# Kernel optimization log

Measured on AMD Instinct MI355X. Metric: run time of the kernel, lower is better.

## Reference

```python
import jax, jax.numpy as jnp
import numpy as np

B, N, D = 16, 4096, 6
NUM_CENTERS, K = 1024, 32
EPS = 1e-5


def setup_inputs() -> dict:
    key = jax.random.key(0)
    ks = jax.random.split(key, 6)
    xyz = jax.random.uniform(ks[0], (B, N, 3), dtype=jnp.float32)
    features = jax.random.normal(ks[1], (B, N, D), dtype=jnp.float32)
    W1 = jax.random.normal(ks[2], (3 + D, 64), dtype=jnp.float32) * 0.1
    W2 = jax.random.normal(ks[3], (64, 64), dtype=jnp.float32) * 0.1
    W3 = jax.random.normal(ks[4], (64, 128), dtype=jnp.float32) * 0.1
    return {
        "xyz": xyz, "features": features,
        "W1": W1, "g1": jnp.ones((64,)), "b1": jnp.zeros((64,)),
        "W2": W2, "g2": jnp.ones((64,)), "b2": jnp.zeros((64,)),
        "W3": W3, "g3": jnp.ones((128,)), "b3": jnp.zeros((128,)),
    }


def square_distance(a, b):
    # a: [B,S,3], b: [B,N,3] -> [B,S,N] squared euclidean distance
    d2 = (jnp.sum(a * a, -1)[:, :, None]
          + jnp.sum(b * b, -1)[:, None, :]
          - 2.0 * jnp.einsum('bsc,bnc->bsn', a, b))
    return jnp.maximum(d2, 0.0)


def farthest_point_sample(xyz, num_centers):
    # xyz: [B,N,3] -> centers_idx: [B,S]. First center fixed at index 0
    # (original uses a random first index; deterministic here).
    Bn = xyz.shape[0]
    batch = jnp.arange(Bn)
    first = jnp.zeros((Bn,), jnp.int32)
    d0 = jnp.sum((xyz - xyz[batch, first][:, None, :]) ** 2, -1)  # [B,N]

    def step(dist_closest, _):
        idx = jnp.argmax(dist_closest, axis=1).astype(jnp.int32)  # [B]
        c = xyz[batch, idx]                                        # [B,3]
        d = jnp.sum((xyz - c[:, None, :]) ** 2, -1)                # [B,N]
        return jnp.minimum(dist_closest, d), idx

    _, rest = jax.lax.scan(step, d0, None, length=num_centers - 1)  # [S-1,B]
    return jnp.concatenate([first[:, None], rest.T], axis=1)        # [B,S]


def gather_bsk(points, idx):
    # points: [B,N,C], idx: [B,S,K] -> [B,S,K,C]
    Bn = points.shape[0]
    return points[jnp.arange(Bn)[:, None, None], idx]


def conv_bn_relu(x, W, g, b):
    # 1x1 conv (channel matmul) + training-mode BatchNorm (biased var) + ReLU
    x = jnp.einsum('bskc,co->bsko', x, W)
    m = jnp.mean(x, axis=(0, 1, 2))
    v = jnp.var(x, axis=(0, 1, 2))
    return jax.nn.relu((x - m) * jax.lax.rsqrt(v + EPS) * g + b)


def reference(xyz, features, W1, g1, b1, W2, g2, b2, W3, g3, b3):
    Bn = xyz.shape[0]
    batch = jnp.arange(Bn)
    centers_idx = farthest_point_sample(xyz, NUM_CENTERS)          # [B,S]
    centers_xyz = xyz[batch[:, None], centers_idx]                  # [B,S,3]

    # kNN grouping: [B,S,N] distance matrix, top-K smallest
    d2 = square_distance(centers_xyz, xyz)
    _, group_idx = jax.lax.top_k(-d2, K)                            # [B,S,K]

    group_xyz = gather_bsk(xyz, group_idx) - centers_xyz[:, :, None, :]
    group_feat = gather_bsk(features, group_idx)
    group = jnp.concatenate([group_xyz, group_feat], axis=-1)       # [B,S,K,3+D]

    x = conv_bn_relu(group, W1, g1, b1)
    x = conv_bn_relu(x, W2, g2, b2)
    x = conv_bn_relu(x, W3, g3, b3)
    centers_features = jnp.max(x, axis=2)                           # [B,S,C_out]
    return centers_xyz, centers_features
```

## Files before the change

kernel.cpp:

```cpp
#include <hip/hip_runtime.h>

#define BN_   16
#define NPTS  4096
#define DFEAT 6
#define SCTR  1024
#define KNN   32
#define RTOT  (BN_*SCTR*KNN)
#define EPSV  1e-5f
#define RNF   524288.0f
#define NREP  64

__device__ __forceinline__ float fmulx(float a, float b){ return __fmul_rn(a,b); }
__device__ __forceinline__ float faddx(float a, float b){ return __fadd_rn(a,b); }
__device__ __forceinline__ float fsubx(float a, float b){ return __fsub_rn(a,b); }
__device__ __forceinline__ float sq3x(float x, float y, float z){
  return faddx(faddx(fmulx(x,x), fmulx(y,y)), fmulx(z,z));
}
__device__ __forceinline__ float dot3fma(float ax, float ay, float az,
                                         float bx, float by, float bz){
  return __fmaf_rn(az, bz, __fmaf_rn(ay, by, __fmul_rn(ax, bx)));
}

__device__ __forceinline__ unsigned fkey(float f){
  unsigned u = __float_as_uint(f);
  return (u & 0x80000000u) ? ~u : (u | 0x80000000u);
}
__device__ __forceinline__ float funkey(unsigned k){
  return (k & 0x80000000u) ? __uint_as_float(k & 0x7fffffffu) : __uint_as_float(~k);
}

template<int CTRL>
__device__ __forceinline__ unsigned dpp_mv(unsigned v){
  return (unsigned)__builtin_amdgcn_update_dpp((int)v, (int)v, CTRL, 0xf, 0xf, false);
}
__device__ __forceinline__ unsigned wave_umax_b(unsigned v){
  unsigned o;
  o=dpp_mv<0x111>(v); v=v>o?v:o;
  o=dpp_mv<0x112>(v); v=v>o?v:o;
  o=dpp_mv<0x114>(v); v=v>o?v:o;
  o=dpp_mv<0x118>(v); v=v>o?v:o;
  o=dpp_mv<0x142>(v); v=v>o?v:o;
  o=dpp_mv<0x143>(v); v=v>o?v:o;
  return (unsigned)__builtin_amdgcn_readlane((int)v, 63);
}
__device__ __forceinline__ unsigned wave_umin_b(unsigned v){
  unsigned o;
  o=dpp_mv<0x111>(v); v=v<o?v:o;
  o=dpp_mv<0x112>(v); v=v<o?v:o;
  o=dpp_mv<0x114>(v); v=v<o?v:o;
  o=dpp_mv<0x118>(v); v=v<o?v:o;
  o=dpp_mv<0x142>(v); v=v<o?v:o;
  o=dpp_mv<0x143>(v); v=v<o?v:o;
  return (unsigned)__builtin_amdgcn_readlane((int)v, 63);
}

__global__ __launch_bounds__(256) void k_fps(const float* __restrict__ xyz,
                                             float* __restrict__ cxyz){
  const int b = blockIdx.x, tid = threadIdx.x;
  const int wave = tid>>6, lane = tid&63;
  const float* X = xyz + (size_t)b*NPTS*3;
  __shared__ float Xl[NPTS*3];
  __shared__ float Cl[SCTR*3];
  __shared__ unsigned long long slot[2][4];
  for(int i=tid;i<NPTS*3;i+=256) Xl[i]=X[i];
  __syncthreads();
  float px[16],py[16],pz[16],mind[16];
  const float c0x=Xl[0], c0y=Xl[1], c0z=Xl[2];
#pragma unroll
  for(int t=0;t<16;t++){
    const int j = lane + 64*(wave*16+t);
    px[t]=Xl[j*3]; py[t]=Xl[j*3+1]; pz[t]=Xl[j*3+2];
    mind[t]=sq3x(fsubx(px[t],c0x), fsubx(py[t],c0y), fsubx(pz[t],c0z));
  }
  if(tid==0){ Cl[0]=c0x; Cl[1]=c0y; Cl[2]=c0z; }
  float bv=-1.0f; int bj=0x7fffffff;
#pragma unroll
  for(int t=0;t<16;t++){
    const int j = lane + 64*(wave*16+t);
    if(mind[t]>bv){ bv=mind[t]; bj=j; }
  }
  for(int it=1; it<SCTR; ++it){
    const unsigned uv = __float_as_uint(bv);
    const unsigned M  = wave_umax_b(uv);
    const unsigned nj = (uv == M) ? ~(unsigned)bj : 0u;
    const unsigned NJ = wave_umax_b(nj);
    if(lane==0) slot[it&1][wave] = ((unsigned long long)M<<32) | NJ;
    __syncthreads();
    unsigned long long k0=slot[it&1][0], k1=slot[it&1][1],
                       k2=slot[it&1][2], k3=slot[it&1][3];
    unsigned long long ka = k0>k1?k0:k1;
    unsigned long long kb = k2>k3?k2:k3;
    unsigned long long kw = ka>kb?ka:kb;
    const int w = (int)(~(unsigned)kw);
    const float cx=Xl[w*3], cy=Xl[w*3+1], cz=Xl[w*3+2];
    if(tid==0){ Cl[it*3]=cx; Cl[it*3+1]=cy; Cl[it*3+2]=cz; }
    bv=-1.0f; bj=0x7fffffff;
#pragma unroll
    for(int t=0;t<16;t++){
      float d = sq3x(fsubx(px[t],cx), fsubx(py[t],cy), fsubx(pz[t],cz));
      float nm = fminf(mind[t], d);
      mind[t]=nm;
      const int j = lane + 64*(wave*16+t);
      if(nm>bv){ bv=nm; bj=j; }
    }
  }
  __syncthreads();
  float* O = cxyz + (size_t)b*SCTR*3;
  for(int i=tid;i<SCTR*3;i+=256) O[i]=Cl[i];
}

__global__ __launch_bounds__(256) void k_select(const float* __restrict__ xyz,
                                                const float* __restrict__ cxyz,
                                                int* __restrict__ gidx){
  const int lane = threadIdx.x & 63;
  const int cid  = blockIdx.x*4 + (threadIdx.x>>6);
  const int b = cid>>10;
  const float* X = xyz + (size_t)b*NPTS*3;
  const float* C = cxyz + (size_t)cid*3;
  const float cx=C[0], cy=C[1], cz=C[2];
  const float a2 = sq3x(cx,cy,cz);
  float d[64];
#pragma unroll
  for(int t=0;t<64;t++){
    int j = lane + (t<<6);
    float x=X[j*3], y=X[j*3+1], z=X[j*3+2];
    float b2 = sq3x(x,y,z);
    float dt = dot3fma(cx,cy,cz, x,y,z);
    float dd = fsubx(faddx(a2,b2), fmulx(2.0f,dt));
    d[t] = fmaxf(dd, 0.0f);
  }
  unsigned long long taken = 0ull;
  int* out = gidx + (size_t)cid*KNN;
#pragma unroll 1
  for(int r=0;r<KNN;r++){
    float mv = 3.0e38f; int mt = 63;
#pragma unroll
    for(int t=0;t<64;t++){
      if(!(taken & (1ull<<t)) && d[t] < mv){ mv = d[t]; mt = t; }
    }
    const unsigned um = __float_as_uint(mv);
    const unsigned Mw = wave_umin_b(um);
    const unsigned jc = (um == Mw) ? (unsigned)(lane + (mt<<6)) : 0xffffffffu;
    const unsigned WJ = wave_umin_b(jc);
    if(lane == (int)(WJ & 63u)){
      out[r] = (int)WJ;
      taken |= (1ull << (WJ >> 6));
    }
  }
}

__device__ __forceinline__ void stage_in(float* INt, int rbase,
                                         const float* __restrict__ xyz,
                                         const float* __restrict__ feat,
                                         const float* __restrict__ cxyz,
                                         const int* __restrict__ gidx){
  const int tid = threadIdx.x;
  const int row = tid>>2, sub = tid&3;
  const int r  = rbase + row;
  const int bb = r>>15, ss=(r>>5)&1023;
  const int idx = gidx[r];
  if(sub==0){
    const float* P = xyz  + ((size_t)bb*NPTS + idx)*3;
    const float* C = cxyz + ((size_t)(bb*SCTR)+ss)*3;
    INt[0*68+row] = P[0]-C[0];
    INt[1*68+row] = P[1]-C[1];
    INt[2*68+row] = P[2]-C[2];
  }else{
    const float* F = feat + ((size_t)bb*NPTS + idx)*6;
    const int c = (sub-1)*2;
    INt[(3+c)*68+row] = F[c];
    INt[(4+c)*68+row] = F[c+1];
  }
}

__device__ __forceinline__ void gemm1(const float* INt, const float* __restrict__ W1,
                                      int rt, int ct, float acc[4][4]){
#pragma unroll
  for(int i=0;i<4;i++)
#pragma unroll
    for(int j=0;j<4;j++) acc[i][j]=0.f;
#pragma unroll
  for(int c=0;c<9;c++){
    const float4 a = *(const float4*)&INt[c*68 + rt*4];
    const float4 w = *(const float4*)&W1[c*64 + ct*4];
    const float av[4]={a.x,a.y,a.z,a.w}, wv[4]={w.x,w.y,w.z,w.w};
#pragma unroll
    for(int i=0;i<4;i++)
#pragma unroll
      for(int j=0;j<4;j++) acc[i][j] += av[i]*wv[j];
  }
}

__device__ __forceinline__ float fold_rep(const float* __restrict__ pstats, int off){
  float s=0.f;
#pragma unroll 8
  for(int c=0;c<NREP;c++) s += pstats[c*512 + off];
  return s;
}

__global__ __launch_bounds__(256) void k_stats1(const float* __restrict__ xyz,
                                                const float* __restrict__ feat,
                                                const float* __restrict__ cxyz,
                                                const int* __restrict__ gidx,
                                                const float* __restrict__ W1,
                                                float* __restrict__ pstats){
  __shared__ __align__(16) float INt[9*68];
  __shared__ float sb[64], qb[64];
  const int tid=threadIdx.x;
  if(tid<64){ sb[tid]=0.f; qb[tid]=0.f; }
  stage_in(INt, blockIdx.x*64, xyz, feat, cxyz, gidx);
  __syncthreads();
  const int rt=tid&15, ct=tid>>4;
  float acc[4][4];
  gemm1(INt, W1, rt, ct, acc);
#pragma unroll
  for(int j=0;j<4;j++){
    float s=0.f, q=0.f;
#pragma unroll
    for(int i=0;i<4;i++){ float v=acc[i][j]; s+=v; q+=v*v; }
    atomicAdd(&sb[ct*4+j], s); atomicAdd(&qb[ct*4+j], q);
  }
  __syncthreads();
  if(tid<64){
    float* ps = pstats + (size_t)(blockIdx.x & (NREP-1))*512;
    atomicAdd(&ps[tid], sb[tid]); atomicAdd(&ps[64+tid], qb[tid]);
  }
}

template<bool WRITEZ>
__device__ __forceinline__ void stats2_body(const float* xyz, const float* feat,
                                            const float* cxyz, const int* gidx,
                                            const float* W1, const float* g1,
                                            const float* b1, const float* __restrict__ W2,
                                            float* pstats, float* Z2){
  __shared__ __align__(16) float INt[9*68];
  __shared__ __align__(16) float A1t[64*68];
  __shared__ float af1A[64], af1B[64];
  __shared__ float sb[64], qb[64];
  const int tid=threadIdx.x;
  if(tid<64){
    float sm = fold_rep(pstats, tid);
    float sq = fold_rep(pstats, 64+tid);
    float m  = sm/RNF;
    float vv = sq/RNF - m*m;
    float A  = rsqrtf(vv+EPSV)*g1[tid];
    af1A[tid]=A; af1B[tid]=b1[tid]-m*A;
    sb[tid]=0.f; qb[tid]=0.f;
  }
  stage_in(INt, blockIdx.x*64, xyz, feat, cxyz, gidx);
  __syncthreads();
  const int rt=tid&15, ct=tid>>4;
  float acc1[4][4];
  gemm1(INt, W1, rt, ct, acc1);
#pragma unroll
  for(int j=0;j<4;j++){
    const int o=ct*4+j; const float A=af1A[o], Bc=af1B[o];
#pragma unroll
    for(int i=0;i<4;i++) A1t[o*68 + rt*4+i] = fmaxf(acc1[i][j]*A+Bc, 0.f);
  }
  __syncthreads();
  float acc2[4][4];
#pragma unroll
  for(int i=0;i<4;i++)
#pragma unroll
    for(int j=0;j<4;j++) acc2[i][j]=0.f;
#pragma unroll
  for(int c=0;c<64;c++){
    const float4 a = *(const float4*)&A1t[c*68 + rt*4];
    const float4 w = *(const float4*)&W2[c*64 + ct*4];
    const float av[4]={a.x,a.y,a.z,a.w}, wv[4]={w.x,w.y,w.z,w.w};
#pragma unroll
    for(int i=0;i<4;i++)
#pragma unroll
      for(int j=0;j<4;j++) acc2[i][j] += av[i]*wv[j];
  }
  if(WRITEZ){
#pragma unroll
    for(int i=0;i<4;i++){
      float4 v = make_float4(acc2[i][0],acc2[i][1],acc2[i][2],acc2[i][3]);
      *(float4*)&Z2[((size_t)blockIdx.x*64 + rt*4+i)*64 + ct*4] = v;
    }
  }
#pragma unroll
  for(int j=0;j<4;j++){
    float s=0.f, q=0.f;
#pragma unroll
    for(int i=0;i<4;i++){ float v=acc2[i][j]; s+=v; q+=v*v; }
    atomicAdd(&sb[ct*4+j], s); atomicAdd(&qb[ct*4+j], q);
  }
  __syncthreads();
  if(tid<64){
    float* ps = pstats + (size_t)(blockIdx.x & (NREP-1))*512;
    atomicAdd(&ps[128+tid], sb[tid]); atomicAdd(&ps[192+tid], qb[tid]);
  }
}

__global__ __launch_bounds__(256) void k_stats2(const float* __restrict__ xyz,
                                                const float* __restrict__ feat,
                                                const float* __restrict__ cxyz,
                                                const int* __restrict__ gidx,
                                                const float* __restrict__ W1,
                                                const float* __restrict__ g1,
                                                const float* __restrict__ b1,
                                                const float* __restrict__ W2,
                                                float* __restrict__ pstats){
  stats2_body<false>(xyz,feat,cxyz,gidx,W1,g1,b1,W2,pstats,nullptr);
}
__global__ __launch_bounds__(256) void k_stats2m(const float* __restrict__ xyz,
                                                 const float* __restrict__ feat,
                                                 const float* __restrict__ cxyz,
                                                 const int* __restrict__ gidx,
                                                 const float* __restrict__ W1,
                                                 const float* __restrict__ g1,
                                                 const float* __restrict__ b1,
                                                 const float* __restrict__ W2,
                                                 float* __restrict__ pstats,
                                                 float* __restrict__ Z2){
  stats2_body<true>(xyz,feat,cxyz,gidx,W1,g1,b1,W2,pstats,Z2);
}

__global__ __launch_bounds__(256) void k_layer3(const float* __restrict__ xyz,
                                                const float* __restrict__ feat,
                                                const float* __restrict__ cxyz,
                                                const int* __restrict__ gidx,
                                                const float* __restrict__ W1,
                                                const float* __restrict__ g1,
                                                const float* __restrict__ b1,
                                                const float* __restrict__ W2,
                                                const float* __restrict__ g2,
                                                const float* __restrict__ b2,
                                                const float* __restrict__ W3,
                                                float* __restrict__ pstats,
                                                float* __restrict__ premax){
  __shared__ __align__(16) float INt[9*68];
  __shared__ __align__(16) float A1t[64*68];
  __shared__ float af1A[64], af1B[64], af2A[64], af2B[64];
  __shared__ unsigned mx[256];
  __shared__ float s3b[256], q3b[256];
  const int tid=threadIdx.x;
  if(tid<64){
    float sm = fold_rep(pstats, tid);
    float sq = fold_rep(pstats, 64+tid);
    float m  = sm/RNF;
    float vv = sq/RNF - m*m;
    float A  = rsqrtf(vv+EPSV)*g1[tid];
    af1A[tid]=A; af1B[tid]=b1[tid]-m*A;
    float sm2 = fold_rep(pstats, 128+tid);
    float sq2 = fold_rep(pstats, 192+tid);
    float m2 = sm2/RNF;
    float v2 = sq2/RNF - m2*m2;
    float A2 = rsqrtf(v2+EPSV)*g2[tid];
    af2A[tid]=A2; af2B[tid]=b2[tid]-m2*A2;
  }
  mx[tid]=0u; s3b[tid]=0.f; q3b[tid]=0.f;
  stage_in(INt, blockIdx.x*64, xyz, feat, cxyz, gidx);
  __syncthreads();
  const int rt=tid&15, ct=tid>>4;
  float acc1[4][4];
  gemm1(INt, W1, rt, ct, acc1);
#pragma unroll
  for(int j=0;j<4;j++){
    const int o=ct*4+j; const float A=af1A[o], Bc=af1B[o];
#pragma unroll
    for(int i=0;i<4;i++) A1t[o*68 + rt*4+i] = fmaxf(acc1[i][j]*A+Bc, 0.f);
  }
  __syncthreads();
  float acc2[4][4];
#pragma unroll
  for(int i=0;i<4;i++)
#pragma unroll
    for(int j=0;j<4;j++) acc2[i][j]=0.f;
#pragma unroll
  for(int c=0;c<64;c++){
    const float4 a = *(const float4*)&A1t[c*68 + rt*4];
    const float4 w = *(const float4*)&W2[c*64 + ct*4];
    const float av[4]={a.x,a.y,a.z,a.w}, wv[4]={w.x,w.y,w.z,w.w};
#pragma unroll
    for(int i=0;i<4;i++)
#pragma unroll
      for(int j=0;j<4;j++) acc2[i][j] += av[i]*wv[j];
  }
  float a2v[4][4];
#pragma unroll
  for(int j=0;j<4;j++){
    const int o=ct*4+j; const float A=af2A[o], Bc=af2B[o];
#pragma unroll
    for(int i=0;i<4;i++) a2v[i][j]=fmaxf(acc2[i][j]*A+Bc, 0.f);
  }
  __syncthreads();
#pragma unroll
  for(int j=0;j<4;j++)
#pragma unroll
    for(int i=0;i<4;i++) A1t[(ct*4+j)*68 + rt*4+i] = a2v[i][j];
  __syncthreads();
  float acc3[4][8];
#pragma unroll
  for(int i=0;i<4;i++)
#pragma unroll
    for(int j=0;j<8;j++) acc3[i][j]=0.f;
#pragma unroll
  for(int c=0;c<64;c++){
    const float4 a  = *(const float4*)&A1t[c*68 + rt*4];
    const float4 w0 = *(const float4*)&W3[c*128 + ct*8];
    const float4 w1 = *(const float4*)&W3[c*128 + ct*8 + 4];
    const float av[4]={a.x,a.y,a.z,a.w};
    const float wv[8]={w0.x,w0.y,w0.z,w0.w,w1.x,w1.y,w1.z,w1.w};
#pragma unroll
    for(int i=0;i<4;i++)
#pragma unroll
      for(int j=0;j<8;j++) acc3[i][j] += av[i]*wv[j];
  }
  const int g = rt>>3;
#pragma unroll
  for(int j=0;j<8;j++){
    const int o=ct*8+j;
    float lm=acc3[0][j], s=0.f, q=0.f;
#pragma unroll
    for(int i=0;i<4;i++){ float v=acc3[i][j]; lm=fmaxf(lm,v); s+=v; q+=v*v; }
    atomicMax(&mx[g*128+o], fkey(lm));
    atomicAdd(&s3b[g*128+o], s);
    atomicAdd(&q3b[g*128+o], q);
  }
  __syncthreads();
  {
    const int gg=tid>>7, o=tid&127;
    const int cid = blockIdx.x*2+gg;
    premax[(size_t)cid*128+o] = funkey(mx[tid]);
  }
  if(tid<128){
    float* ps = pstats + (size_t)(blockIdx.x & (NREP-1))*512;
    atomicAdd(&ps[256+tid], s3b[tid]+s3b[128+tid]);
    atomicAdd(&ps[384+tid], q3b[tid]+q3b[128+tid]);
  }
}

__global__ __launch_bounds__(256) void k_layer3z(const float* __restrict__ Z2,
                                                 const float* __restrict__ g2,
                                                 const float* __restrict__ b2,
                                                 const float* __restrict__ W3,
                                                 float* __restrict__ pstats,
                                                 float* __restrict__ premax){
  __shared__ __align__(16) float A2t[64*68];
  __shared__ float af2A[64], af2B[64];
  __shared__ unsigned mx[256];
  __shared__ float s3b[256], q3b[256];
  const int tid=threadIdx.x;
  if(tid<64){
    float sm2 = fold_rep(pstats, 128+tid);
    float sq2 = fold_rep(pstats, 192+tid);
    float m2 = sm2/RNF;
    float v2 = sq2/RNF - m2*m2;
    float A2 = rsqrtf(v2+EPSV)*g2[tid];
    af2A[tid]=A2; af2B[tid]=b2[tid]-m2*A2;
  }
  mx[tid]=0u; s3b[tid]=0.f; q3b[tid]=0.f;
  __syncthreads();
  {
    const int row = tid>>2, cq = (tid&3)*16;
    const float* zr = Z2 + ((size_t)blockIdx.x*64 + row)*64 + cq;
    const float4 z0 = *(const float4*)(zr);
    const float4 z1 = *(const float4*)(zr+4);
    const float4 z2 = *(const float4*)(zr+8);
    const float4 z3 = *(const float4*)(zr+12);
    const float zz[16]={z0.x,z0.y,z0.z,z0.w, z1.x,z1.y,z1.z,z1.w,
                        z2.x,z2.y,z2.z,z2.w, z3.x,z3.y,z3.z,z3.w};
#pragma unroll
    for(int u=0;u<16;u++){
      const int c = cq+u;
      A2t[c*68+row] = fmaxf(zz[u]*af2A[c]+af2B[c], 0.f);
    }
  }
  __syncthreads();
  const int rt=tid&15, ct=tid>>4;
  float acc3[4][8];
#pragma unroll
  for(int i=0;i<4;i++)
#pragma unroll
    for(int j=0;j<8;j++) acc3[i][j]=0.f;
#pragma unroll
  for(int c=0;c<64;c++){
    const float4 a  = *(const float4*)&A2t[c*68 + rt*4];
    const float4 w0 = *(const float4*)&W3[c*128 + ct*8];
    const float4 w1 = *(const float4*)&W3[c*128 + ct*8 + 4];
    const float av[4]={a.x,a.y,a.z,a.w};
    const float wv[8]={w0.x,w0.y,w0.z,w0.w,w1.x,w1.y,w1.z,w1.w};
#pragma unroll
    for(int i=0;i<4;i++)
#pragma unroll
      for(int j=0;j<8;j++) acc3[i][j] += av[i]*wv[j];
  }
  const int g = rt>>3;
#pragma unroll
  for(int j=0;j<8;j++){
    const int o=ct*8+j;
    float lm=acc3[0][j], s=0.f, q=0.f;
#pragma unroll
    for(int i=0;i<4;i++){ float v=acc3[i][j]; lm=fmaxf(lm,v); s+=v; q+=v*v; }
    atomicMax(&mx[g*128+o], fkey(lm));
    atomicAdd(&s3b[g*128+o], s);
    atomicAdd(&q3b[g*128+o], q);
  }
  __syncthreads();
  {
    const int gg=tid>>7, o=tid&127;
    const int cid = blockIdx.x*2+gg;
    premax[(size_t)cid*128+o] = funkey(mx[tid]);
  }
  if(tid<128){
    float* ps = pstats + (size_t)(blockIdx.x & (NREP-1))*512;
    atomicAdd(&ps[256+tid], s3b[tid]+s3b[128+tid]);
    atomicAdd(&ps[384+tid], q3b[tid]+q3b[128+tid]);
  }
}

__global__ __launch_bounds__(256) void k_red3(const float* __restrict__ pstats,
                                              float* __restrict__ cstats){
  const int t = threadIdx.x;
  cstats[t] = fold_rep(pstats, 256+t);
}

__global__ __launch_bounds__(256) void k_final(const float* __restrict__ cstats,
                                               const float* __restrict__ g3,
                                               const float* __restrict__ b3,
                                               float* __restrict__ outf){
  const int i = blockIdx.x*256 + threadIdx.x;
  const int o = i & 127;
  float m  = cstats[o]/RNF;
  float vv = cstats[128+o]/RNF - m*m;
  float A  = rsqrtf(vv+EPSV)*g3[o];
  float Bc = b3[o]-m*A;
  float v  = outf[i];
  outf[i] = fmaxf(v*A+Bc, 0.f);
}

extern "C" void kernel_launch(void* const* d_in, const int* in_sizes, int n_in,
                              void* d_out, int out_size, void* d_ws, size_t ws_size,
                              hipStream_t stream){
  const float* xyz  = (const float*)d_in[0];
  const float* feat = (const float*)d_in[1];
  const float* W1   = (const float*)d_in[2];
  const float* g1   = (const float*)d_in[3];
  const float* b1   = (const float*)d_in[4];
  const float* W2   = (const float*)d_in[5];
  const float* g2   = (const float*)d_in[6];
  const float* b2   = (const float*)d_in[7];
  const float* W3   = (const float*)d_in[8];
  const float* g3   = (const float*)d_in[9];
  const float* b3   = (const float*)d_in[10];
  float* out  = (float*)d_out;
  float* cxyz = out;
  float* outf = out + 16*1024*3;
  float* pstats = (float*)d_ws;
  float* cstats = (float*)((char*)d_ws + 131072);
  int*   gidx   = (int*)((char*)d_ws + 133120);
  float* Z2     = (float*)((char*)d_ws + 133120 + (size_t)RTOT*4);
  const size_t need = 133120 + (size_t)RTOT*4 + (size_t)RTOT*64*4;
  const bool fast = (ws_size >= need);

  hipMemsetAsync(pstats, 0, (size_t)NREP*512*sizeof(float), stream);
  k_fps   <<<16,   256,  0, stream>>>(xyz, cxyz);
  k_select<<<4096, 256,  0, stream>>>(xyz, cxyz, gidx);
  k_stats1<<<8192, 256,  0, stream>>>(xyz, feat, cxyz, gidx, W1, pstats);
  if(fast){
    k_stats2m<<<8192, 256, 0, stream>>>(xyz, feat, cxyz, gidx, W1, g1, b1, W2, pstats, Z2);
    k_layer3z<<<8192, 256, 0, stream>>>(Z2, g2, b2, W3, pstats, outf);
  }else{
    k_stats2 <<<8192, 256, 0, stream>>>(xyz, feat, cxyz, gidx, W1, g1, b1, W2, pstats);
    k_layer3 <<<8192, 256, 0, stream>>>(xyz, feat, cxyz, gidx, W1, g1, b1, W2, g2, b2, W3, pstats, outf);
  }
  k_red3  <<<1,    256,  0, stream>>>(pstats, cstats);
  k_final <<<8192, 256,  0, stream>>>(cstats, g3, b3, outf);
}
```

Before: 1.667 ms.

## Cache layer-1 activations in workspace and pass FPS centroid coords via LDS

In the fast path, the first stats kernel now writes the layer-1 pre-activations to a workspace buffer. The second stats kernel reads that buffer instead of re-gathering neighbours and recomputing the first GEMM, and it overwrites the same buffer in place with the layer-2 output. Separately, FPS no longer copies the whole point cloud into shared memory: the winning lane of each wave publishes its point coordinates through a small LDS slot alongside the argmax key. This trades an extra 128MB write-and-read of intermediates for removing the gather and GEMM1 recompute, and it shortens the serial FPS step by dropping the dependent indexed LDS load.

Result: slower. 1.992 ms (+19.5%).

```diff
diff --git a/kernel.cpp b/kernel.cpp
--- a/kernel.cpp
+++ b/kernel.cpp
@@ -59,49 +59,53 @@
   const int b = blockIdx.x, tid = threadIdx.x;
   const int wave = tid>>6, lane = tid&63;
   const float* X = xyz + (size_t)b*NPTS*3;
-  __shared__ float Xl[NPTS*3];
   __shared__ float Cl[SCTR*3];
   __shared__ unsigned long long slot[2][4];
-  for(int i=tid;i<NPTS*3;i+=256) Xl[i]=X[i];
-  __syncthreads();
+  __shared__ __align__(16) float4 cslot[2][4];
   float px[16],py[16],pz[16],mind[16];
-  const float c0x=Xl[0], c0y=Xl[1], c0z=Xl[2];
+  const float c0x=X[0], c0y=X[1], c0z=X[2];
 #pragma unroll
   for(int t=0;t<16;t++){
     const int j = lane + 64*(wave*16+t);
-    px[t]=Xl[j*3]; py[t]=Xl[j*3+1]; pz[t]=Xl[j*3+2];
+    px[t]=X[j*3]; py[t]=X[j*3+1]; pz[t]=X[j*3+2];
     mind[t]=sq3x(fsubx(px[t],c0x), fsubx(py[t],c0y), fsubx(pz[t],c0z));
   }
   if(tid==0){ Cl[0]=c0x; Cl[1]=c0y; Cl[2]=c0z; }
-  float bv=-1.0f; int bj=0x7fffffff;
+  float bv=-1.0f; int bj=0x7fffffff, bt=0;
 #pragma unroll
   for(int t=0;t<16;t++){
     const int j = lane + 64*(wave*16+t);
-    if(mind[t]>bv){ bv=mind[t]; bj=j; }
+    if(mind[t]>bv){ bv=mind[t]; bj=j; bt=t; }
   }
   for(int it=1; it<SCTR; ++it){
     const unsigned uv = __float_as_uint(bv);
     const unsigned M  = wave_umax_b(uv);
     const unsigned nj = (uv == M) ? ~(unsigned)bj : 0u;
     const unsigned NJ = wave_umax_b(nj);
-    if(lane==0) slot[it&1][wave] = ((unsigned long long)M<<32) | NJ;
+    if(~(unsigned)bj == NJ){
+      slot[it&1][wave]  = ((unsigned long long)M<<32) | NJ;
+      cslot[it&1][wave] = make_float4(px[bt], py[bt], pz[bt], 0.f);
+    }
     __syncthreads();
-    unsigned long long k0=slot[it&1][0], k1=slot[it&1][1],
-                       k2=slot[it&1][2], k3=slot[it&1][3];
-    unsigned long long ka = k0>k1?k0:k1;
-    unsigned long long kb = k2>k3?k2:k3;
-    unsigned long long kw = ka>kb?ka:kb;
-    const int w = (int)(~(unsigned)kw);
-    const float cx=Xl[w*3], cy=Xl[w*3+1], cz=Xl[w*3+2];
+    const unsigned long long k0=slot[it&1][0], k1=slot[it&1][1],
+                             k2=slot[it&1][2], k3=slot[it&1][3];
+    const float4 q0=cslot[it&1][0], q1=cslot[it&1][1],
+                 q2=cslot[it&1][2], q3=cslot[it&1][3];
+    unsigned long long ka, kb, kw; float4 ca, cb, cw;
+    if(k0>k1){ ka=k0; ca=q0; } else { ka=k1; ca=q1; }
+    if(k2>k3){ kb=k2; cb=q2; } else { kb=k3; cb=q3; }
+    if(ka>kb){ kw=ka; cw=ca; } else { kw=kb; cw=cb; }
+    (void)kw;
+    const float cx=cw.x, cy=cw.y, cz=cw.z;
     if(tid==0){ Cl[it*3]=cx; Cl[it*3+1]=cy; Cl[it*3+2]=cz; }
-    bv=-1.0f; bj=0x7fffffff;
+    bv=-1.0f; bj=0x7fffffff; bt=0;
 #pragma unroll
     for(int t=0;t<16;t++){
       float d = sq3x(fsubx(px[t],cx), fsubx(py[t],cy), fsubx(pz[t],cz));
       float nm = fminf(mind[t], d);
       mind[t]=nm;
       const int j = lane + 64*(wave*16+t);
-      if(nm>bv){ bv=nm; bj=j; }
+      if(nm>bv){ bv=nm; bj=j; bt=t; }
     }
   }
   __syncthreads();
@@ -227,13 +231,46 @@
   }
 }
 
-template<bool WRITEZ>
-__device__ __forceinline__ void stats2_body(const float* xyz, const float* feat,
-                                            const float* cxyz, const int* gidx,
-                                            const float* W1, const float* g1,
-                                            const float* b1, const float* __restrict__ W2,
-                                            float* pstats, float* Z2){
+__global__ __launch_bounds__(256) void k_stats1z(const float* __restrict__ xyz,
+                                                 const float* __restrict__ feat,
+                                                 const float* __restrict__ cxyz,
+                                                 const int* __restrict__ gidx,
+                                                 const float* __restrict__ W1,
+                                                 float* __restrict__ pstats,
+                                                 float* __restrict__ Z1){
   __shared__ __align__(16) float INt[9*68];
+  __shared__ float sb[64], qb[64];
+  const int tid=threadIdx.x;
+  if(tid<64){ sb[tid]=0.f; qb[tid]=0.f; }
+  stage_in(INt, blockIdx.x*64, xyz, feat, cxyz, gidx);
+  __syncthreads();
+  const int rt=tid&15, ct=tid>>4;
+  float acc[4][4];
+  gemm1(INt, W1, rt, ct, acc);
+#pragma unroll
+  for(int i=0;i<4;i++){
+    float4 v = make_float4(acc[i][0],acc[i][1],acc[i][2],acc[i][3]);
+    *(float4*)&Z1[((size_t)blockIdx.x*64 + rt*4+i)*64 + ct*4] = v;
+  }
+#pragma unroll
+  for(int j=0;j<4;j++){
+    float s=0.f, q=0.f;
+#pragma unroll
+    for(int i=0;i<4;i++){ float v=acc[i][j]; s+=v; q+=v*v; }
+    atomicAdd(&sb[ct*4+j], s); atomicAdd(&qb[ct*4+j], q);
+  }
+  __syncthreads();
+  if(tid<64){
+    float* ps = pstats + (size_t)(blockIdx.x & (NREP-1))*512;
+    atomicAdd(&ps[tid], sb[tid]); atomicAdd(&ps[64+tid], qb[tid]);
+  }
+}
+
+__global__ __launch_bounds__(256) void k_stats2z(const float* __restrict__ g1,
+                                                 const float* __restrict__ b1,
+                                                 const float* __restrict__ W2,
+                                                 float* __restrict__ pstats,
+                                                 float* __restrict__ Z){
   __shared__ __align__(16) float A1t[64*68];
   __shared__ float af1A[64], af1B[64];
   __shared__ float sb[64], qb[64];
@@ -247,18 +284,24 @@
     af1A[tid]=A; af1B[tid]=b1[tid]-m*A;
     sb[tid]=0.f; qb[tid]=0.f;
   }
-  stage_in(INt, blockIdx.x*64, xyz, feat, cxyz, gidx);
+  __syncthreads();
+  {
+    const int row = tid>>2, cq = (tid&3)*16;
+    const float* zr = Z + ((size_t)blockIdx.x*64 + row)*64 + cq;
+    const float4 z0 = *(const float4*)(zr);
+    const float4 z1 = *(const float4*)(zr+4);
+    const float4 z2 = *(const float4*)(zr+8);
+    const float4 z3 = *(const float4*)(zr+12);
+    const float zz[16]={z0.x,z0.y,z0.z,z0.w, z1.x,z1.y,z1.z,z1.w,
+                        z2.x,z2.y,z2.z,z2.w, z3.x,z3.y,z3.z,z3.w};
+#pragma unroll
+    for(int u=0;u<16;u++){
+      const int c = cq+u;
+      A1t[c*68+row] = fmaxf(zz[u]*af1A[c]+af1B[c], 0.f);
+    }
+  }
   __syncthreads();
   const int rt=tid&15, ct=tid>>4;
-  float acc1[4][4];
-  gemm1(INt, W1, rt, ct, acc1);
-#pragma unroll
-  for(int j=0;j<4;j++){
-    const int o=ct*4+j; const float A=af1A[o], Bc=af1B[o];
-#pragma unroll
-    for(int i=0;i<4;i++) A1t[o*68 + rt*4+i] = fmaxf(acc1[i][j]*A+Bc, 0.f);
-  }
-  __syncthreads();
   float acc2[4][4];
 #pragma unroll
   for(int i=0;i<4;i++)
@@ -274,12 +317,10 @@
 #pragma unroll
       for(int j=0;j<4;j++) acc2[i][j] += av[i]*wv[j];
   }
-  if(WRITEZ){
-#pragma unroll
-    for(int i=0;i<4;i++){
-      float4 v = make_float4(acc2[i][0],acc2[i][1],acc2[i][2],acc2[i][3]);
-      *(float4*)&Z2[((size_t)blockIdx.x*64 + rt*4+i)*64 + ct*4] = v;
-    }
+#pragma unroll
+  for(int i=0;i<4;i++){
+    float4 v = make_float4(acc2[i][0],acc2[i][1],acc2[i][2],acc2[i][3]);
+    *(float4*)&Z[((size_t)blockIdx.x*64 + rt*4+i)*64 + ct*4] = v;
   }
 #pragma unroll
   for(int j=0;j<4;j++){
@@ -304,19 +345,59 @@
                                                 const float* __restrict__ b1,
                                                 const float* __restrict__ W2,
                                                 float* __restrict__ pstats){
-  stats2_body<false>(xyz,feat,cxyz,gidx,W1,g1,b1,W2,pstats,nullptr);
-}
-__global__ __launch_bounds__(256) void k_stats2m(const float* __restrict__ xyz,
-                                                 const float* __restrict__ feat,
-                                                 const float* __restrict__ cxyz,
-                                                 const int* __restrict__ gidx,
-                                                 const float* __restrict__ W1,
-                                                 const float* __restrict__ g1,
-                                                 const float* __restrict__ b1,
-                                                 const float* __restrict__ W2,
-                                                 float* __restrict__ pstats,
-                                                 float* __restrict__ Z2){
-  stats2_body<true>(xyz,feat,cxyz,gidx,W1,g1,b1,W2,pstats,Z2);
+  __shared__ __align__(16) float INt[9*68];
+  __shared__ __align__(16) float A1t[64*68];
+  __shared__ float af1A[64], af1B[64];
+  __shared__ float sb[64], qb[64];
+  const int tid=threadIdx.x;
+  if(tid<64){
+    float sm = fold_rep(pstats, tid);
+    float sq = fold_rep(pstats, 64+tid);
+    float m  = sm/RNF;
+    float vv = sq/RNF - m*m;
+    float A  = rsqrtf(vv+EPSV)*g1[tid];
+    af1A[tid]=A; af1B[tid]=b1[tid]-m*A;
+    sb[tid]=0.f; qb[tid]=0.f;
+  }
+  stage_in(INt, blockIdx.x*64, xyz, feat, cxyz, gidx);
+  __syncthreads();
+  const int rt=tid&15, ct=tid>>4;
+  float acc1[4][4];
+  gemm1(INt, W1, rt, ct, acc1);
+#pragma unroll
+  for(int j=0;j<4;j++){
+    const int o=ct*4+j; const float A=af1A[o], Bc=af1B[o];
+#pragma unroll
+    for(int i=0;i<4;i++) A1t[o*68 + rt*4+i] = fmaxf(acc1[i][j]*A+Bc, 0.f);
+  }
+  __syncthreads();
+  float acc2[4][4];
+#pragma unroll
+  for(int i=0;i<4;i++)
+#pragma unroll
+    for(int j=0;j<4;j++) acc2[i][j]=0.f;
+#pragma unroll
+  for(int c=0;c<64;c++){
+    const float4 a = *(const float4*)&A1t[c*68 + rt*4];
+    const float4 w = *(const float4*)&W2[c*64 + ct*4];
+    const float av[4]={a.x,a.y,a.z,a.w}, wv[4]={w.x,w.y,w.z,w.w};
+#pragma unroll
+    for(int i=0;i<4;i++)
+#pragma unroll
+      for(int j=0;j<4;j++) acc2[i][j] += av[i]*wv[j];
+  }
+#pragma unroll
+  for(int j=0;j<4;j++){
+    float s=0.f, q=0.f;
+#pragma unroll
+    for(int i=0;i<4;i++){ float v=acc2[i][j]; s+=v; q+=v*v; }
+    atomicAdd(&sb[ct*4+j], s); atomicAdd(&qb[ct*4+j], q);
+  }
+  __syncthreads();
+  if(tid<64){
+    float* ps = pstats + (size_t)(blockIdx.x & (NREP-1))*512;
+    atomicAdd(&ps[128+tid], sb[tid]); atomicAdd(&ps[192+tid], qb[tid]);
+  }
 }
 
 __global__ __launch_bounds__(256) void k_layer3(const float* __restrict__ xyz,
@@ -553,18 +634,19 @@
   float* pstats = (float*)d_ws;
   float* cstats = (float*)((char*)d_ws + 131072);
   int*   gidx   = (int*)((char*)d_ws + 133120);
-  float* Z2     = (float*)((char*)d_ws + 133120 + (size_t)RTOT*4);
+  float* Zbuf   = (float*)((char*)d_ws + 133120 + (size_t)RTOT*4);
   const size_t need = 133120 + (size_t)RTOT*4 + (size_t)RTOT*64*4;
   const bool fast = (ws_size >= need);
 
   hipMemsetAsync(pstats, 0, (size_t)NREP*512*sizeof(float), stream);
   k_fps   <<<16,   256,  0, stream>>>(xyz, cxyz);
   k_select<<<4096, 256,  0, stream>>>(xyz, cxyz, gidx);
-  k_stats1<<<8192, 256,  0, stream>>>(xyz, feat, cxyz, gidx, W1, pstats);
   if(fast){
-    k_stats2m<<<8192, 256, 0, stream>>>(xyz, feat, cxyz, gidx, W1, g1, b1, W2, pstats, Z2);
-    k_layer3z<<<8192, 256, 0, stream>>>(Z2, g2, b2, W3, pstats, outf);
+    k_stats1z<<<8192, 256, 0, stream>>>(xyz, feat, cxyz, gidx, W1, pstats, Zbuf);
+    k_stats2z<<<8192, 256, 0, stream>>>(g1, b1, W2, pstats, Zbuf);
+    k_layer3z<<<8192, 256, 0, stream>>>(Zbuf, g2, b2, W3, pstats, outf);
   }else{
+    k_stats1 <<<8192, 256, 0, stream>>>(xyz, feat, cxyz, gidx, W1, pstats);
     k_stats2 <<<8192, 256, 0, stream>>>(xyz, feat, cxyz, gidx, W1, g1, b1, W2, pstats);
     k_layer3 <<<8192, 256, 0, stream>>>(xyz, feat, cxyz, gidx, W1, g1, b1, W2, g2, b2, W3, pstats, outf);
   }
```
